# Optimization experiments

Hardware: AMD Instinct MI355X
Metric: run time of the kernel (lower is better)

Reference implementation:

```python
import jax, jax.numpy as jnp
import numpy as np

B, H, S, D = 2, 16, 2048, 64


def setup_inputs() -> dict:
    key = jax.random.key(0)
    kq, kk, kv = jax.random.split(key, 3)
    q = jax.random.normal(kq, (B, H, S, D), dtype=jnp.float32)
    k = jax.random.normal(kk, (B, H, S, D), dtype=jnp.float32)
    v = jax.random.normal(kv, (B, H, S, D), dtype=jnp.float32)
    # look-ahead (causal) mask: 1 where attention is NOT allowed (future positions)
    mask = 1.0 - jnp.tril(jnp.ones((S, S), dtype=jnp.float32))
    mask = mask[None, None, :, :]  # broadcastable to (B, H, S, S)
    return {"q": q, "k": k, "v": v, "mask": mask}


def reference(q, k, v, mask):
    # scores: (B, H, Sq, Sk)
    dk = jnp.asarray(q.shape[-1], dtype=q.dtype)
    logits = jnp.einsum("bhqd,bhkd->bhqk", q, k) / jnp.sqrt(dk)
    logits = logits + mask * (-1e9)
    attn = jax.nn.softmax(logits, axis=-1)
    # dropout rate 0.0 / inference mode -> identity
    out = jnp.einsum("bhqk,bhkd->bhqd", attn, v)
    return out, attn
```

## Files before the change

### kernel.cpp

```cpp
#include <hip/hip_runtime.h>


typedef __attribute__((ext_vector_type(4))) float f32x4;
typedef __attribute__((ext_vector_type(8))) short bf16x8;

#define S_LEN 2048
#define D_DIM 64
#define LDK   72
#define SCALE2 0.18033688f

__device__ __forceinline__ void bar_lds() {
  asm volatile("s_waitcnt lgkmcnt(0)" ::: "memory");
  __builtin_amdgcn_s_barrier();
}

__device__ __forceinline__ unsigned int f2bf1(float f) {
  unsigned int u = __float_as_uint(f);
  return (u + 0x7FFFu + ((u >> 16) & 1u)) >> 16;
}
__device__ __forceinline__ unsigned long long pack4bf(float a, float b, float c, float d) {
  unsigned int lo = f2bf1(a) | (f2bf1(b) << 16);
  unsigned int hi = f2bf1(c) | (f2bf1(d) << 16);
  return (unsigned long long)lo | ((unsigned long long)hi << 32);
}

__global__ __launch_bounds__(256, 2)
void attn_fused(const float* __restrict__ Qg, const float* __restrict__ Kg,
                const float* __restrict__ Vg, float* __restrict__ Og,
                float* __restrict__ Ag)
{
  __shared__ __attribute__((aligned(16))) unsigned short qs[64 * LDK];
  __shared__ __attribute__((aligned(16))) unsigned short ks[2][64 * LDK];
  __shared__ __attribute__((aligned(16))) unsigned short vs[2][64 * LDK];
  __shared__ __attribute__((aligned(16))) unsigned short ps[4 * 16 * LDK];

  const int tid  = threadIdx.x;
  const int w    = tid >> 6;
  const int l15  = tid & 15;
  const int lg   = (tid >> 4) & 3;
  const int bh   = blockIdx.x & 31;
  const int pj   = blockIdx.x >> 5;

  const float* qb = Qg + (size_t)bh * S_LEN * D_DIM;
  const float* kb = Kg + (size_t)bh * S_LEN * D_DIM;
  const float* vb = Vg + (size_t)bh * S_LEN * D_DIM;
  float* ob = Og + (size_t)bh * S_LEN * D_DIM;
  float* ab = Ag + (size_t)bh * S_LEN * S_LEN;

  unsigned short* pw = ps + w * 16 * LDK;

  for (int sel = 0; sel < 2; ++sel) {
    const int jq  = sel ? (31 - pj) : pj;
    const int q0  = jq << 6;
    const int T   = jq + 1;
    const int qr0 = q0 + w * 16 + lg * 4;

    bar_lds();
#pragma unroll
    for (int jj = 0; jj < 4; ++jj) {
      int f = tid + jj * 256;
      int row = f >> 4, dg = f & 15;
      float4 v = *(const float4*)(qb + (q0 + row) * D_DIM + dg * 4);
      *(unsigned long long*)(qs + row * LDK + dg * 4) = pack4bf(v.x, v.y, v.z, v.w);
    }
    bar_lds();
    const bf16x8 qf0 = *(const bf16x8*)(qs + (w * 16 + l15) * LDK + lg * 8);
    const bf16x8 qf1 = *(const bf16x8*)(qs + (w * 16 + l15) * LDK + 32 + lg * 8);

    float lsum[4] = {0.f, 0.f, 0.f, 0.f};
#pragma unroll
    for (int jj = 0; jj < 4; ++jj) {
      int f = tid + jj * 256;
      int row = f >> 4, dg = f & 15;
      float4 v = *(const float4*)(kb + row * D_DIM + dg * 4);
      *(unsigned long long*)(ks[0] + row * LDK + dg * 4) = pack4bf(v.x, v.y, v.z, v.w);
    }
    bar_lds();
    int cur = 0;
    for (int t = 0; t < T; ++t) {
      const int kt = t << 6;
      const bool pf = (t + 1 < T);
      float4 kl[4];
      if (pf) {
#pragma unroll
        for (int jj = 0; jj < 4; ++jj) {
          int f = tid + jj * 256;
          int row = f >> 4, dg = f & 15;
          kl[jj] = *(const float4*)(kb + (kt + 64 + row) * D_DIM + dg * 4);
        }
      }
      const unsigned short* kcur = ks[cur];
#pragma unroll
      for (int kbk = 0; kbk < 4; ++kbk) {
        const bf16x8 kf0 = *(const bf16x8*)(kcur + (kbk * 16 + l15) * LDK + lg * 8);
        const bf16x8 kf1 = *(const bf16x8*)(kcur + (kbk * 16 + l15) * LDK + 32 + lg * 8);
        f32x4 s = {0.f, 0.f, 0.f, 0.f};
        s = __builtin_amdgcn_mfma_f32_16x16x32_bf16(qf0, kf0, s, 0, 0, 0);
        s = __builtin_amdgcn_mfma_f32_16x16x32_bf16(qf1, kf1, s, 0, 0, 0);
        const int kc = kt + kbk * 16 + l15;
#pragma unroll
        for (int r = 0; r < 4; ++r)
          lsum[r] += (kc <= qr0 + r) ? exp2f(s[r] * SCALE2) : 0.f;
      }
      if (pf) {
#pragma unroll
        for (int jj = 0; jj < 4; ++jj) {
          int f = tid + jj * 256;
          int row = f >> 4, dg = f & 15;
          *(unsigned long long*)(ks[cur ^ 1] + row * LDK + dg * 4) =
              pack4bf(kl[jj].x, kl[jj].y, kl[jj].z, kl[jj].w);
        }
      }
      bar_lds();
      cur ^= 1;
    }
#pragma unroll
    for (int m = 1; m < 16; m <<= 1) {
#pragma unroll
      for (int r = 0; r < 4; ++r) lsum[r] += __shfl_xor(lsum[r], m, 64);
    }
    float ri[4];
#pragma unroll
    for (int r = 0; r < 4; ++r) ri[r] = 1.f / lsum[r];

    f32x4 o[4];
#pragma unroll
    for (int d = 0; d < 4; ++d) o[d] = (f32x4){0.f, 0.f, 0.f, 0.f};

#pragma unroll
    for (int jj = 0; jj < 4; ++jj) {
      int f = tid + jj * 256;
      int row = f >> 4, dg = f & 15;
      float4 v = *(const float4*)(kb + row * D_DIM + dg * 4);
      *(unsigned long long*)(ks[0] + row * LDK + dg * 4) = pack4bf(v.x, v.y, v.z, v.w);
    }
    {
      const int kb4 = tid >> 4, db4 = tid & 15;
      const float* vsrc = vb + (kb4 * 4) * D_DIM + db4 * 4;
      float4 r0 = *(const float4*)(vsrc);
      float4 r1 = *(const float4*)(vsrc + D_DIM);
      float4 r2 = *(const float4*)(vsrc + 2 * D_DIM);
      float4 r3 = *(const float4*)(vsrc + 3 * D_DIM);
      *(unsigned long long*)(vs[0] + (db4 * 4 + 0) * LDK + kb4 * 4) = pack4bf(r0.x, r1.x, r2.x, r3.x);
      *(unsigned long long*)(vs[0] + (db4 * 4 + 1) * LDK + kb4 * 4) = pack4bf(r0.y, r1.y, r2.y, r3.y);
      *(unsigned long long*)(vs[0] + (db4 * 4 + 2) * LDK + kb4 * 4) = pack4bf(r0.z, r1.z, r2.z, r3.z);
      *(unsigned long long*)(vs[0] + (db4 * 4 + 3) * LDK + kb4 * 4) = pack4bf(r0.w, r1.w, r2.w, r3.w);
    }
    bar_lds();
    cur = 0;
    for (int t = 0; t < T; ++t) {
      const int kt = t << 6;
      const bool pf = (t + 1 < T);
      float4 kl[4], v0, v1, v2, v3;
      if (pf) {
#pragma unroll
        for (int jj = 0; jj < 4; ++jj) {
          int f = tid + jj * 256;
          int row = f >> 4, dg = f & 15;
          kl[jj] = *(const float4*)(kb + (kt + 64 + row) * D_DIM + dg * 4);
        }
        const int kb4 = tid >> 4, db4 = tid & 15;
        const float* vsrc = vb + (kt + 64 + kb4 * 4) * D_DIM + db4 * 4;
        v0 = *(const float4*)(vsrc);
        v1 = *(const float4*)(vsrc + D_DIM);
        v2 = *(const float4*)(vsrc + 2 * D_DIM);
        v3 = *(const float4*)(vsrc + 3 * D_DIM);
      }
      const unsigned short* kcur = ks[cur];
#pragma unroll
      for (int kbk = 0; kbk < 4; ++kbk) {
        const bf16x8 kf0 = *(const bf16x8*)(kcur + (kbk * 16 + l15) * LDK + lg * 8);
        const bf16x8 kf1 = *(const bf16x8*)(kcur + (kbk * 16 + l15) * LDK + 32 + lg * 8);
        f32x4 s = {0.f, 0.f, 0.f, 0.f};
        s = __builtin_amdgcn_mfma_f32_16x16x32_bf16(qf0, kf0, s, 0, 0, 0);
        s = __builtin_amdgcn_mfma_f32_16x16x32_bf16(qf1, kf1, s, 0, 0, 0);
        const int kc = kt + kbk * 16 + l15;
#pragma unroll
        for (int r = 0; r < 4; ++r) {
          float p = (kc <= qr0 + r) ? exp2f(s[r] * SCALE2) * ri[r] : 0.f;
          pw[(lg * 4 + r) * LDK + kbk * 16 + l15] = (unsigned short)f2bf1(p);
        }
      }
      asm volatile("s_waitcnt lgkmcnt(0)" ::: "memory");

#pragma unroll
      for (int jj = 0; jj < 4; ++jj) {
        const int row = jj * 4 + lg;
        uint2 pk2 = *(const uint2*)(pw + row * LDK + l15 * 4);
        f32x4 fv;
        fv.x = __uint_as_float((pk2.x & 0xFFFFu) << 16);
        fv.y = __uint_as_float(pk2.x & 0xFFFF0000u);
        fv.z = __uint_as_float((pk2.y & 0xFFFFu) << 16);
        fv.w = __uint_as_float(pk2.y & 0xFFFF0000u);
        __builtin_nontemporal_store(fv,
          (f32x4*)(ab + (size_t)(q0 + w * 16 + row) * S_LEN + kt + l15 * 4));
      }

      const bf16x8 pa0 = *(const bf16x8*)(pw + l15 * LDK + lg * 8);
      const bf16x8 pa1 = *(const bf16x8*)(pw + l15 * LDK + 32 + lg * 8);
      const unsigned short* vcur = vs[cur];
#pragma unroll
      for (int d = 0; d < 4; ++d) {
        const bf16x8 vf0 = *(const bf16x8*)(vcur + (d * 16 + l15) * LDK + lg * 8);
        const bf16x8 vf1 = *(const bf16x8*)(vcur + (d * 16 + l15) * LDK + 32 + lg * 8);
        o[d] = __builtin_amdgcn_mfma_f32_16x16x32_bf16(pa0, vf0, o[d], 0, 0, 0);
        o[d] = __builtin_amdgcn_mfma_f32_16x16x32_bf16(pa1, vf1, o[d], 0, 0, 0);
      }
      if (pf) {
#pragma unroll
        for (int jj = 0; jj < 4; ++jj) {
          int f = tid + jj * 256;
          int row = f >> 4, dg = f & 15;
          *(unsigned long long*)(ks[cur ^ 1] + row * LDK + dg * 4) =
              pack4bf(kl[jj].x, kl[jj].y, kl[jj].z, kl[jj].w);
        }
        const int kb4 = tid >> 4, db4 = tid & 15;
        *(unsigned long long*)(vs[cur ^ 1] + (db4 * 4 + 0) * LDK + kb4 * 4) = pack4bf(v0.x, v1.x, v2.x, v3.x);
        *(unsigned long long*)(vs[cur ^ 1] + (db4 * 4 + 1) * LDK + kb4 * 4) = pack4bf(v0.y, v1.y, v2.y, v3.y);
        *(unsigned long long*)(vs[cur ^ 1] + (db4 * 4 + 2) * LDK + kb4 * 4) = pack4bf(v0.z, v1.z, v2.z, v3.z);
        *(unsigned long long*)(vs[cur ^ 1] + (db4 * 4 + 3) * LDK + kb4 * 4) = pack4bf(v0.w, v1.w, v2.w, v3.w);
      }
      bar_lds();
      cur ^= 1;
    }

    {
      const f32x4 z = (f32x4){0.f, 0.f, 0.f, 0.f};
#pragma unroll
      for (int jj = 0; jj < 4; ++jj) {
        const int qrow = q0 + w * 16 + jj * 4 + lg;
        float* rp = ab + (size_t)qrow * S_LEN;
        for (int c = q0 + 64 + l15 * 4; c < S_LEN; c += 64)
          __builtin_nontemporal_store(z, (f32x4*)(rp + c));
      }
    }

#pragma unroll
    for (int r = 0; r < 4; ++r) {
      float* rp = ob + (size_t)(qr0 + r) * D_DIM + l15;
      __builtin_nontemporal_store(o[0][r], rp);
      __builtin_nontemporal_store(o[1][r], rp + 16);
      __builtin_nontemporal_store(o[2][r], rp + 32);
      __builtin_nontemporal_store(o[3][r], rp + 48);
    }
  }
}

extern "C" void kernel_launch(void* const* d_in, const int* in_sizes, int n_in,
                              void* d_out, int out_size, void* d_ws, size_t ws_size,
                              hipStream_t stream) {
  (void)in_sizes; (void)n_in; (void)d_ws; (void)ws_size; (void)out_size;
  const float* q = (const float*)d_in[0];
  const float* k = (const float*)d_in[1];
  const float* v = (const float*)d_in[2];
  float* out  = (float*)d_out;
  float* attn = out + (size_t)2 * 16 * 2048 * 64;
  attn_fused<<<dim3(512), dim3(256), 0, stream>>>(q, k, v, out, attn);
}
```

Before: 157.5 us.

## Split attention into row-sum/zero-fill kernel and probability-store kernel

```diff
diff --git a/kernel.cpp b/kernel.cpp
--- a/kernel.cpp
+++ b/kernel.cpp
@@ -9,11 +9,6 @@
 #define LDK   72
 #define SCALE2 0.18033688f
 
-__device__ __forceinline__ void bar_lds() {
-  asm volatile("s_waitcnt lgkmcnt(0)" ::: "memory");
-  __builtin_amdgcn_s_barrier();
-}
-
 __device__ __forceinline__ unsigned int f2bf1(float f) {
   unsigned int u = __float_as_uint(f);
   return (u + 0x7FFFu + ((u >> 16) & 1u)) >> 16;
@@ -25,14 +20,11 @@
 }
 
 __global__ __launch_bounds__(256, 2)
-void attn_fused(const float* __restrict__ Qg, const float* __restrict__ Kg,
-                const float* __restrict__ Vg, float* __restrict__ Og,
-                float* __restrict__ Ag)
+void rowsum_zfill(const float* __restrict__ Qg, const float* __restrict__ Kg,
+                  float* __restrict__ Ri, float* __restrict__ Ag)
 {
   __shared__ __attribute__((aligned(16))) unsigned short qs[64 * LDK];
   __shared__ __attribute__((aligned(16))) unsigned short ks[2][64 * LDK];
-  __shared__ __attribute__((aligned(16))) unsigned short vs[2][64 * LDK];
-  __shared__ __attribute__((aligned(16))) unsigned short ps[4 * 16 * LDK];
 
   const int tid  = threadIdx.x;
   const int w    = tid >> 6;
@@ -43,11 +35,8 @@
 
   const float* qb = Qg + (size_t)bh * S_LEN * D_DIM;
   const float* kb = Kg + (size_t)bh * S_LEN * D_DIM;
-  const float* vb = Vg + (size_t)bh * S_LEN * D_DIM;
-  float* ob = Og + (size_t)bh * S_LEN * D_DIM;
-  float* ab = Ag + (size_t)bh * S_LEN * S_LEN;
-
-  unsigned short* pw = ps + w * 16 * LDK;
+  float* rib = Ri + (size_t)bh * S_LEN;
+  float* ab  = Ag + (size_t)bh * S_LEN * S_LEN;
 
   for (int sel = 0; sel < 2; ++sel) {
     const int jq  = sel ? (31 - pj) : pj;
@@ -55,7 +44,7 @@
     const int T   = jq + 1;
     const int qr0 = q0 + w * 16 + lg * 4;
 
-    bar_lds();
+    __syncthreads();
 #pragma unroll
     for (int jj = 0; jj < 4; ++jj) {
       int f = tid + jj * 256;
@@ -63,19 +52,18 @@
       float4 v = *(const float4*)(qb + (q0 + row) * D_DIM + dg * 4);
       *(unsigned long long*)(qs + row * LDK + dg * 4) = pack4bf(v.x, v.y, v.z, v.w);
     }
-    bar_lds();
+#pragma unroll
+    for (int jj = 0; jj < 4; ++jj) {
+      int f = tid + jj * 256;
+      int row = f >> 4, dg = f & 15;
+      float4 v = *(const float4*)(kb + row * D_DIM + dg * 4);
+      *(unsigned long long*)(ks[0] + row * LDK + dg * 4) = pack4bf(v.x, v.y, v.z, v.w);
+    }
+    __syncthreads();
     const bf16x8 qf0 = *(const bf16x8*)(qs + (w * 16 + l15) * LDK + lg * 8);
     const bf16x8 qf1 = *(const bf16x8*)(qs + (w * 16 + l15) * LDK + 32 + lg * 8);
 
     float lsum[4] = {0.f, 0.f, 0.f, 0.f};
-#pragma unroll
-    for (int jj = 0; jj < 4; ++jj) {
-      int f = tid + jj * 256;
-      int row = f >> 4, dg = f & 15;
-      float4 v = *(const float4*)(kb + row * D_DIM + dg * 4);
-      *(unsigned long long*)(ks[0] + row * LDK + dg * 4) = pack4bf(v.x, v.y, v.z, v.w);
-    }
-    bar_lds();
     int cur = 0;
     for (int t = 0; t < T; ++t) {
       const int kt = t << 6;
@@ -111,7 +99,7 @@
               pack4bf(kl[jj].x, kl[jj].y, kl[jj].z, kl[jj].w);
         }
       }
-      bar_lds();
+      __syncthreads();
       cur ^= 1;
     }
 #pragma unroll
@@ -119,14 +107,64 @@
 #pragma unroll
       for (int r = 0; r < 4; ++r) lsum[r] += __shfl_xor(lsum[r], m, 64);
     }
-    float ri[4];
-#pragma unroll
-    for (int r = 0; r < 4; ++r) ri[r] = 1.f / lsum[r];
-
-    f32x4 o[4];
-#pragma unroll
-    for (int d = 0; d < 4; ++d) o[d] = (f32x4){0.f, 0.f, 0.f, 0.f};
-
+    if (l15 == 0) {
+#pragma unroll
+      for (int r = 0; r < 4; ++r) rib[qr0 + r] = 1.f / lsum[r];
+    }
+
+    {
+      const f32x4 z = (f32x4){0.f, 0.f, 0.f, 0.f};
+#pragma unroll
+      for (int jj = 0; jj < 4; ++jj) {
+        const int qrow = q0 + w * 16 + jj * 4 + lg;
+        float* rp = ab + (size_t)qrow * S_LEN;
+        for (int c = q0 + 64 + l15 * 4; c < S_LEN; c += 64)
+          __builtin_nontemporal_store(z, (f32x4*)(rp + c));
+      }
+    }
+  }
+}
+
+__global__ __launch_bounds__(256, 2)
+void attn_store(const float* __restrict__ Qg, const float* __restrict__ Kg,
+                const float* __restrict__ Vg, const float* __restrict__ Ri,
+                float* __restrict__ Og, float* __restrict__ Ag)
+{
+  __shared__ __attribute__((aligned(16))) unsigned short qs[64 * LDK];
+  __shared__ __attribute__((aligned(16))) unsigned short ks[2][64 * LDK];
+  __shared__ __attribute__((aligned(16))) unsigned short vs[2][64 * LDK];
+  __shared__ __attribute__((aligned(16))) unsigned short ps[4 * 16 * LDK];
+
+  const int tid  = threadIdx.x;
+  const int w    = tid >> 6;
+  const int l15  = tid & 15;
+  const int lg   = (tid >> 4) & 3;
+  const int bh   = blockIdx.x & 31;
+  const int pj   = blockIdx.x >> 5;
+
+  const float* qb = Qg + (size_t)bh * S_LEN * D_DIM;
+  const float* kb = Kg + (size_t)bh * S_LEN * D_DIM;
+  const float* vb = Vg + (size_t)bh * S_LEN * D_DIM;
+  const float* rib = Ri + (size_t)bh * S_LEN;
+  float* ob = Og + (size_t)bh * S_LEN * D_DIM;
+  float* ab = Ag + (size_t)bh * S_LEN * S_LEN;
+
+  unsigned short* pw = ps + w * 16 * LDK;
+
+  for (int sel = 0; sel < 2; ++sel) {
+    const int jq  = sel ? (31 - pj) : pj;
+    const int q0  = jq << 6;
+    const int T   = jq + 1;
+    const int qr0 = q0 + w * 16 + lg * 4;
+
+    __syncthreads();
+#pragma unroll
+    for (int jj = 0; jj < 4; ++jj) {
+      int f = tid + jj * 256;
+      int row = f >> 4, dg = f & 15;
+      float4 v = *(const float4*)(qb + (q0 + row) * D_DIM + dg * 4);
+      *(unsigned long long*)(qs + row * LDK + dg * 4) = pack4bf(v.x, v.y, v.z, v.w);
+    }
 #pragma unroll
     for (int jj = 0; jj < 4; ++jj) {
       int f = tid + jj * 256;
@@ -146,8 +184,18 @@
       *(unsigned long long*)(vs[0] + (db4 * 4 + 2) * LDK + kb4 * 4) = pack4bf(r0.z, r1.z, r2.z, r3.z);
       *(unsigned long long*)(vs[0] + (db4 * 4 + 3) * LDK + kb4 * 4) = pack4bf(r0.w, r1.w, r2.w, r3.w);
     }
-    bar_lds();
-    cur = 0;
+    float ri[4];
+#pragma unroll
+    for (int r = 0; r < 4; ++r) ri[r] = rib[qr0 + r];
+    __syncthreads();
+    const bf16x8 qf0 = *(const bf16x8*)(qs + (w * 16 + l15) * LDK + lg * 8);
+    const bf16x8 qf1 = *(const bf16x8*)(qs + (w * 16 + l15) * LDK + 32 + lg * 8);
+
+    f32x4 o[4];
+#pragma unroll
+    for (int d = 0; d < 4; ++d) o[d] = (f32x4){0.f, 0.f, 0.f, 0.f};
+
+    int cur = 0;
     for (int t = 0; t < T; ++t) {
       const int kt = t << 6;
       const bool pf = (t + 1 < T);
@@ -178,23 +226,11 @@
 #pragma unroll
         for (int r = 0; r < 4; ++r) {
           float p = (kc <= qr0 + r) ? exp2f(s[r] * SCALE2) * ri[r] : 0.f;
+          __builtin_nontemporal_store(p, ab + (size_t)(qr0 + r) * S_LEN + kc);
           pw[(lg * 4 + r) * LDK + kbk * 16 + l15] = (unsigned short)f2bf1(p);
         }
       }
       asm volatile("s_waitcnt lgkmcnt(0)" ::: "memory");
-
-#pragma unroll
-      for (int jj = 0; jj < 4; ++jj) {
-        const int row = jj * 4 + lg;
-        uint2 pk2 = *(const uint2*)(pw + row * LDK + l15 * 4);
-        f32x4 fv;
-        fv.x = __uint_as_float((pk2.x & 0xFFFFu) << 16);
-        fv.y = __uint_as_float(pk2.x & 0xFFFF0000u);
-        fv.z = __uint_as_float((pk2.y & 0xFFFFu) << 16);
-        fv.w = __uint_as_float(pk2.y & 0xFFFF0000u);
-        __builtin_nontemporal_store(fv,
-          (f32x4*)(ab + (size_t)(q0 + w * 16 + row) * S_LEN + kt + l15 * 4));
-      }
 
       const bf16x8 pa0 = *(const bf16x8*)(pw + l15 * LDK + lg * 8);
       const bf16x8 pa1 = *(const bf16x8*)(pw + l15 * LDK + 32 + lg * 8);
@@ -220,19 +256,8 @@
         *(unsigned long long*)(vs[cur ^ 1] + (db4 * 4 + 2) * LDK + kb4 * 4) = pack4bf(v0.z, v1.z, v2.z, v3.z);
         *(unsigned long long*)(vs[cur ^ 1] + (db4 * 4 + 3) * LDK + kb4 * 4) = pack4bf(v0.w, v1.w, v2.w, v3.w);
       }
-      bar_lds();
+      __syncthreads();
       cur ^= 1;
-    }
-
-    {
-      const f32x4 z = (f32x4){0.f, 0.f, 0.f, 0.f};
-#pragma unroll
-      for (int jj = 0; jj < 4; ++jj) {
-        const int qrow = q0 + w * 16 + jj * 4 + lg;
-        float* rp = ab + (size_t)qrow * S_LEN;
-        for (int c = q0 + 64 + l15 * 4; c < S_LEN; c += 64)
-          __builtin_nontemporal_store(z, (f32x4*)(rp + c));
-      }
     }
 
 #pragma unroll
@@ -249,11 +274,13 @@
 extern "C" void kernel_launch(void* const* d_in, const int* in_sizes, int n_in,
                               void* d_out, int out_size, void* d_ws, size_t ws_size,
                               hipStream_t stream) {
-  (void)in_sizes; (void)n_in; (void)d_ws; (void)ws_size; (void)out_size;
+  (void)in_sizes; (void)n_in; (void)ws_size; (void)out_size;
   const float* q = (const float*)d_in[0];
   const float* k = (const float*)d_in[1];
   const float* v = (const float*)d_in[2];
   float* out  = (float*)d_out;
   float* attn = out + (size_t)2 * 16 * 2048 * 64;
-  attn_fused<<<dim3(512), dim3(256), 0, stream>>>(q, k, v, out, attn);
-}
+  float* ri   = (float*)d_ws;
+  rowsum_zfill<<<dim3(512), dim3(256), 0, stream>>>(q, k, ri, attn);
+  attn_store <<<dim3(512), dim3(256), 0, stream>>>(q, k, v, ri, out, attn);
+}
```

Result: slower. 212.3 us (+34.8%).

## Load Q and K fragments directly from global into registers in the row-sum pass

Applied to the files above, without the earlier changes.

```diff
diff --git a/kernel.cpp b/kernel.cpp
--- a/kernel.cpp
+++ b/kernel.cpp
@@ -9,11 +9,6 @@
 #define LDK   72
 #define SCALE2 0.18033688f
 
-__device__ __forceinline__ void bar_lds() {
-  asm volatile("s_waitcnt lgkmcnt(0)" ::: "memory");
-  __builtin_amdgcn_s_barrier();
-}
-
 __device__ __forceinline__ unsigned int f2bf1(float f) {
   unsigned int u = __float_as_uint(f);
   return (u + 0x7FFFu + ((u >> 16) & 1u)) >> 16;
@@ -22,6 +17,12 @@
   unsigned int lo = f2bf1(a) | (f2bf1(b) << 16);
   unsigned int hi = f2bf1(c) | (f2bf1(d) << 16);
   return (unsigned long long)lo | ((unsigned long long)hi << 32);
+}
+__device__ __forceinline__ bf16x8 pack8bf(float4 a, float4 b) {
+  union { unsigned long long u[2]; bf16x8 v; } x;
+  x.u[0] = pack4bf(a.x, a.y, a.z, a.w);
+  x.u[1] = pack4bf(b.x, b.y, b.z, b.w);
+  return x.v;
 }
 
 __global__ __launch_bounds__(256, 2)
@@ -29,7 +30,6 @@
                 const float* __restrict__ Vg, float* __restrict__ Og,
                 float* __restrict__ Ag)
 {
-  __shared__ __attribute__((aligned(16))) unsigned short qs[64 * LDK];
   __shared__ __attribute__((aligned(16))) unsigned short ks[2][64 * LDK];
   __shared__ __attribute__((aligned(16))) unsigned short vs[2][64 * LDK];
   __shared__ __attribute__((aligned(16))) unsigned short ps[4 * 16 * LDK];
@@ -55,45 +55,38 @@
     const int T   = jq + 1;
     const int qr0 = q0 + w * 16 + lg * 4;
 
-    bar_lds();
-#pragma unroll
-    for (int jj = 0; jj < 4; ++jj) {
-      int f = tid + jj * 256;
-      int row = f >> 4, dg = f & 15;
-      float4 v = *(const float4*)(qb + (q0 + row) * D_DIM + dg * 4);
-      *(unsigned long long*)(qs + row * LDK + dg * 4) = pack4bf(v.x, v.y, v.z, v.w);
-    }
-    bar_lds();
-    const bf16x8 qf0 = *(const bf16x8*)(qs + (w * 16 + l15) * LDK + lg * 8);
-    const bf16x8 qf1 = *(const bf16x8*)(qs + (w * 16 + l15) * LDK + 32 + lg * 8);
-
+    const float* qrp = qb + (size_t)(q0 + w * 16 + l15) * D_DIM + lg * 8;
+    const bf16x8 qf0 = pack8bf(*(const float4*)(qrp),      *(const float4*)(qrp + 4));
+    const bf16x8 qf1 = pack8bf(*(const float4*)(qrp + 32), *(const float4*)(qrp + 36));
+
+    float4 kc0[8], kc1[8];
+#pragma unroll
+    for (int kbk = 0; kbk < 4; ++kbk) {
+      const float* kp = kb + (size_t)(kbk * 16 + l15) * D_DIM + lg * 8;
+      kc0[2 * kbk]     = *(const float4*)(kp);
+      kc0[2 * kbk + 1] = *(const float4*)(kp + 4);
+      kc1[2 * kbk]     = *(const float4*)(kp + 32);
+      kc1[2 * kbk + 1] = *(const float4*)(kp + 36);
+    }
     float lsum[4] = {0.f, 0.f, 0.f, 0.f};
-#pragma unroll
-    for (int jj = 0; jj < 4; ++jj) {
-      int f = tid + jj * 256;
-      int row = f >> 4, dg = f & 15;
-      float4 v = *(const float4*)(kb + row * D_DIM + dg * 4);
-      *(unsigned long long*)(ks[0] + row * LDK + dg * 4) = pack4bf(v.x, v.y, v.z, v.w);
-    }
-    bar_lds();
-    int cur = 0;
     for (int t = 0; t < T; ++t) {
       const int kt = t << 6;
       const bool pf = (t + 1 < T);
-      float4 kl[4];
-      if (pf) {
-#pragma unroll
-        for (int jj = 0; jj < 4; ++jj) {
-          int f = tid + jj * 256;
-          int row = f >> 4, dg = f & 15;
-          kl[jj] = *(const float4*)(kb + (kt + 64 + row) * D_DIM + dg * 4);
-        }
-      }
-      const unsigned short* kcur = ks[cur];
+      float4 kn0[8], kn1[8];
+      if (pf) {
+#pragma unroll
+        for (int kbk = 0; kbk < 4; ++kbk) {
+          const float* kp = kb + (size_t)(kt + 64 + kbk * 16 + l15) * D_DIM + lg * 8;
+          kn0[2 * kbk]     = *(const float4*)(kp);
+          kn0[2 * kbk + 1] = *(const float4*)(kp + 4);
+          kn1[2 * kbk]     = *(const float4*)(kp + 32);
+          kn1[2 * kbk + 1] = *(const float4*)(kp + 36);
+        }
+      }
 #pragma unroll
       for (int kbk = 0; kbk < 4; ++kbk) {
-        const bf16x8 kf0 = *(const bf16x8*)(kcur + (kbk * 16 + l15) * LDK + lg * 8);
-        const bf16x8 kf1 = *(const bf16x8*)(kcur + (kbk * 16 + l15) * LDK + 32 + lg * 8);
+        const bf16x8 kf0 = pack8bf(kc0[2 * kbk].x == kc0[2 * kbk].x ? kc0[2 * kbk] : kc0[2 * kbk], kc0[2 * kbk + 1]);
+        const bf16x8 kf1 = pack8bf(kc1[2 * kbk], kc1[2 * kbk + 1]);
         f32x4 s = {0.f, 0.f, 0.f, 0.f};
         s = __builtin_amdgcn_mfma_f32_16x16x32_bf16(qf0, kf0, s, 0, 0, 0);
         s = __builtin_amdgcn_mfma_f32_16x16x32_bf16(qf1, kf1, s, 0, 0, 0);
@@ -104,15 +97,8 @@
       }
       if (pf) {
 #pragma unroll
-        for (int jj = 0; jj < 4; ++jj) {
-          int f = tid + jj * 256;
-          int row = f >> 4, dg = f & 15;
-          *(unsigned long long*)(ks[cur ^ 1] + row * LDK + dg * 4) =
-              pack4bf(kl[jj].x, kl[jj].y, kl[jj].z, kl[jj].w);
-        }
-      }
-      bar_lds();
-      cur ^= 1;
+        for (int i = 0; i < 8; ++i) { kc0[i] = kn0[i]; kc1[i] = kn1[i]; }
+      }
     }
 #pragma unroll
     for (int m = 1; m < 16; m <<= 1) {
@@ -146,8 +132,8 @@
       *(unsigned long long*)(vs[0] + (db4 * 4 + 2) * LDK + kb4 * 4) = pack4bf(r0.z, r1.z, r2.z, r3.z);
       *(unsigned long long*)(vs[0] + (db4 * 4 + 3) * LDK + kb4 * 4) = pack4bf(r0.w, r1.w, r2.w, r3.w);
     }
-    bar_lds();
-    cur = 0;
+    __syncthreads();
+    int cur = 0;
     for (int t = 0; t < T; ++t) {
       const int kt = t << 6;
       const bool pf = (t + 1 < T);
@@ -220,7 +206,7 @@
         *(unsigned long long*)(vs[cur ^ 1] + (db4 * 4 + 2) * LDK + kb4 * 4) = pack4bf(v0.z, v1.z, v2.z, v3.z);
         *(unsigned long long*)(vs[cur ^ 1] + (db4 * 4 + 3) * LDK + kb4 * 4) = pack4bf(v0.w, v1.w, v2.w, v3.w);
       }
-      bar_lds();
+      __syncthreads();
       cur ^= 1;
     }
 
```

Measured after the change: 209.4 us. 1.33x slower.
